# Optimization experiments

Measured on AMD Instinct MI355X. Metric: run time of the kernel, lower is better.

## Reference

```python
import jax, jax.numpy as jnp
import numpy as np
from itertools import combinations

# ---- G(3,0,1) projective geometric algebra tables (blade order: grades 0..4, lexicographic) ----

def _build_tables():
    blades = [c for g in range(5) for c in combinations(range(4), g)]
    index = {b: i for i, b in enumerate(blades)}
    def mul(a, b, e0_sq):
        lst = list(a) + list(b)
        sign = 1
        for i in range(len(lst)):
            for j in range(len(lst) - 1 - i):
                if lst[j] > lst[j + 1]:
                    lst[j], lst[j + 1] = lst[j + 1], lst[j]
                    sign = -sign
        out, i = [], 0
        while i < len(lst):
            if i + 1 < len(lst) and lst[i] == lst[i + 1]:
                if lst[i] == 0:
                    sign *= e0_sq  # e0^2 = 0 in PGA geometric product
                i += 2
            else:
                out.append(lst[i]); i += 1
        return tuple(out), sign
    GP = np.zeros((16, 16, 16), np.float32)
    WEDGE = np.zeros((16, 16, 16), np.float32)
    for a in blades:
        for b in blades:
            bl, s = mul(a, b, 0)
            if s != 0:
                GP[index[a], index[b], index[bl]] += s
            if not (set(a) & set(b)):
                bl, s = mul(a, b, 1)
                WEDGE[index[a], index[b], index[bl]] += s
    D = np.zeros((16, 16), np.float32)
    for a in blades:
        c = tuple(sorted(set(range(4)) - set(a)))
        bl, s = mul(a, c, 1)  # e_a ^ e_c = s * e0123
        D[index[c], index[a]] = s
    Dinv = np.linalg.inv(D).astype(np.float32)
    # 9 Pin(3,0,1)-equivariant linear basis maps: 5 grade projections + 4 left-mult by e0
    B = np.zeros((9, 16, 16), np.float32)
    for i, a in enumerate(blades):
        B[len(a), i, i] = 1.0
        if 0 not in a:
            tgt = tuple(sorted((0,) + a))
            B[5 + len(a), index[tgt], i] = 1.0
    inner_idx = np.array([i for i, a in enumerate(blades) if 0 not in a])  # invariant inner product skips e0 blades
    return (jnp.asarray(GP), jnp.asarray(WEDGE), jnp.asarray(D), jnp.asarray(Dinv), jnp.asarray(B), jnp.asarray(inner_idx))

GP_T, WEDGE_T, DUAL, DUAL_INV, BASIS, INNER_IDX = _build_tables()
N_HEADS = 8  # gatr SelfAttentionConfig default


def equi_linear(x, W):
    # x: [..., in_ch, 16], W: [out_ch, in_ch, 9] -> [..., out_ch, 16]
    return jnp.einsum('...ik,oib,bjk->...oj', x, W, BASIS)


def equi_norm(x, eps=1e-6):
    sq = jnp.sum(jnp.take(x, INNER_IDX, axis=-1) ** 2, axis=-1)      # [..., C]
    factor = jnp.mean(sq, axis=-1, keepdims=True)[..., None]          # [..., 1, 1]
    return x * jax.lax.rsqrt(factor + eps)


def geometric_product(x, y):
    return jnp.einsum('...i,...j,ijk->...k', x, y, GP_T)


def equi_join(x, y):
    xd = jnp.einsum('ji,...i->...j', DUAL, x)
    yd = jnp.einsum('ji,...i->...j', DUAL, y)
    w = jnp.einsum('...i,...j,ijk->...k', xd, yd, WEDGE_T)
    return jnp.einsum('ji,...i->...j', DUAL_INV, w)


def attention(x, Wq, Wk, Wv, Wo):
    Bb, N, C, _ = x.shape
    ch = C // N_HEADS
    def split(h):
        return h.reshape(Bb, N, N_HEADS, ch, 16).transpose(0, 2, 1, 3, 4)  # [B,H,N,ch,16]
    q = split(equi_linear(x, Wq))
    k = split(equi_linear(x, Wk))
    v = split(equi_linear(x, Wv))
    qi = jnp.take(q, INNER_IDX, axis=-1)
    ki = jnp.take(k, INNER_IDX, axis=-1)
    logits = jnp.einsum('bhnck,bhmck->bhnm', qi, ki) / np.float32(np.sqrt(8 * ch))
    att = jax.nn.softmax(logits, axis=-1)
    out = jnp.einsum('bhnm,bhmck->bhnck', att, v)
    out = out.transpose(0, 2, 1, 3, 4).reshape(Bb, N, C, 16)
    return equi_linear(out, Wo)


def geo_mlp(x, Wl, Wr, Wm):
    C = x.shape[-2]
    half = C // 2
    left = equi_linear(x, Wl)
    right = equi_linear(x, Wr)
    gp = geometric_product(left[..., :half, :], right[..., :half, :])
    jn = equi_join(left[..., half:, :], right[..., half:, :])
    h = jnp.concatenate([gp, jn], axis=-2)
    h = h * jax.nn.gelu(h[..., 0:1], approximate=False)  # scalar-gated GELU
    return equi_linear(h, Wm)


def embed_point(p):
    # PGA point: homogeneous trivector, e123 coefficient 1
    z = jnp.zeros(p.shape[:-1] + (16,), p.dtype)
    z = z.at[..., 11].set(p[..., 2])
    z = z.at[..., 12].set(-p[..., 1])
    z = z.at[..., 13].set(p[..., 0])
    z = z.at[..., 14].set(1.0)
    return z


def reference(points, W_in, Wq, Wk, Wv, Wo, Wl, Wr, Wm, W_out):
    x = embed_point(points)[..., None, :]   # [B, N, 1, 16]
    x = equi_linear(x, W_in)                # [B, N, C, 16]
    def block(xc, p):
        wq, wk, wv, wo, wl, wr, wm = p
        xc = xc + attention(equi_norm(xc), wq, wk, wv, wo)
        xc = xc + geo_mlp(equi_norm(xc), wl, wr, wm)
        return xc, None
    x, _ = jax.lax.scan(block, x, (Wq, Wk, Wv, Wo, Wl, Wr, Wm))
    out = equi_linear(x, W_out)             # [B, N, 1, 16]
    return jnp.mean(out[..., 0], axis=(1, 2))  # [B]


def setup_inputs():
    key = jax.random.key(0)
    ks = jax.random.split(key, 12)
    B, N, C, L = 1, 2048, 16, 10
    def w(k, o, i):
        return jax.random.normal(k, (o, i, 9), jnp.float32) / np.float32(np.sqrt(9.0 * i))
    def wl(k, o, i):
        return jax.random.normal(k, (L, o, i, 9), jnp.float32) / np.float32(np.sqrt(9.0 * i))
    return {
        'points': jax.random.normal(ks[0], (B, N, 3), jnp.float32),
        'W_in': w(ks[1], C, 1),
        'Wq': wl(ks[2], C, C), 'Wk': wl(ks[3], C, C), 'Wv': wl(ks[4], C, C),
        'Wo': wl(ks[5], C, C), 'Wl': wl(ks[6], C, C), 'Wr': wl(ks[7], C, C),
        'Wm': wl(ks[8], C, C), 'W_out': w(ks[9], 1, C),
    }
```

## Files before the change

kernel.cpp:

```cpp
#include <hip/hip_runtime.h>
#include <hip/hip_bf16.h>
#include <math.h>

#define NTOK 2048

typedef short short8v __attribute__((ext_vector_type(8)));
typedef short short4v __attribute__((ext_vector_type(4)));
typedef float f32x4 __attribute__((ext_vector_type(4)));
typedef unsigned u32x4 __attribute__((ext_vector_type(4)));

__device__ __forceinline__ unsigned short f2bf(float x){
  unsigned u = __float_as_uint(x);
  u += 0x7fff + ((u>>16)&1);
  return (unsigned short)(u>>16);
}
__device__ __forceinline__ unsigned pack_bf2(float a, float b){
  __hip_bfloat162 h = __float22bfloat162_rn(float2{a,b});
  return *reinterpret_cast<unsigned*>(&h);
}

struct GEnt { unsigned char i, j, k; signed char s; };

constexpr int IDX2MASK[16] = {0,1,2,4,8,3,5,9,6,10,12,7,11,13,14,15};
constexpr int MASK2IDX[16] = {0,1,2,5,3,6,8,11,4,7,9,12,10,13,14,15};

constexpr int rsign(int a, int b){
  int cnt=0;
  for(int i=0;i<4;++i) if((b>>i)&1) for(int j=i+1;j<4;++j) if((a>>j)&1) cnt++;
  return (cnt&1)?-1:1;
}

struct GPTab { GEnt e[192]; };
constexpr GPTab make_gp(){
  GPTab t{}; int n=0;
  for(int ia=0; ia<16; ++ia) for(int ib=0; ib<16; ++ib){
    int a=IDX2MASK[ia], b=IDX2MASK[ib];
    if(a&b&1) continue;
    t.e[n].i=(unsigned char)ia; t.e[n].j=(unsigned char)ib;
    t.e[n].k=(unsigned char)MASK2IDX[a^b]; t.e[n].s=(signed char)rsign(a,b);
    ++n;
  }
  return t;
}
static constexpr GPTab GP_TAB = make_gp();

struct JTab { GEnt e[81]; };
constexpr JTab make_join(){
  JTab t{}; int n=0;
  for(int ia=0; ia<16; ++ia) for(int ib=0; ib<16; ++ib){
    int a=IDX2MASK[ia], b=IDX2MASK[ib];
    if((a|b)!=15) continue;
    int ca=(~a)&15, cb=(~b)&15, k=a&b, ck=(~k)&15;
    int s = rsign(a,ca)*rsign(b,cb)*rsign(ca,cb)*rsign(k,ck);
    t.e[n].i=(unsigned char)ia; t.e[n].j=(unsigned char)ib;
    t.e[n].k=(unsigned char)MASK2IDX[k]; t.e[n].s=(signed char)s;
    ++n;
  }
  return t;
}
static constexpr JTab J_TAB = make_join();

constexpr int INNER[8] = {0,2,3,4,8,9,10,14};

__device__ __forceinline__ void apply_gp(float* o, const float* a, const float* b){
#pragma unroll
  for(int n=0;n<192;++n){
    const float s = (float)GP_TAB.e[n].s;
    o[GP_TAB.e[n].k] = fmaf(s*a[GP_TAB.e[n].i], b[GP_TAB.e[n].j], o[GP_TAB.e[n].k]);
  }
}
__device__ __forceinline__ void apply_join(float* o, const float* a, const float* b){
#pragma unroll
  for(int n=0;n<81;++n){
    const float s = (float)J_TAB.e[n].s;
    o[J_TAB.e[n].k] = fmaf(s*a[J_TAB.e[n].i], b[J_TAB.e[n].j], o[J_TAB.e[n].k]);
  }
}

__device__ __forceinline__ void elin_row(float acc[16], const float* xin, const float* w0p){
#pragma unroll
  for(int j=0;j<16;++j) acc[j]=0.0f;
#pragma unroll
  for(int i=0;i<16;++i){
    const float* w = w0p + i*9;
    const float4* xp = (const float4*)(xin + i*16);
    float4 A=xp[0], B=xp[1], Cc=xp[2], D=xp[3];
    float w0=w[0],w1=w[1],w2=w[2],w3=w[3],w4=w[4],w5=w[5],w6=w[6],w7=w[7],w8=w[8];
    acc[0] = fmaf(w0, A.x,  acc[0]);
    acc[1] = fmaf(w1, A.y,  acc[1]);
    acc[2] = fmaf(w1, A.z,  acc[2]);
    acc[3] = fmaf(w1, A.w,  acc[3]);
    acc[4] = fmaf(w1, B.x,  acc[4]);
    acc[5] = fmaf(w2, B.y,  acc[5]);
    acc[6] = fmaf(w2, B.z,  acc[6]);
    acc[7] = fmaf(w2, B.w,  acc[7]);
    acc[8] = fmaf(w2, Cc.x, acc[8]);
    acc[9] = fmaf(w2, Cc.y, acc[9]);
    acc[10]= fmaf(w2, Cc.z, acc[10]);
    acc[11]= fmaf(w3, Cc.w, acc[11]);
    acc[12]= fmaf(w3, D.x,  acc[12]);
    acc[13]= fmaf(w3, D.y,  acc[13]);
    acc[14]= fmaf(w3, D.z,  acc[14]);
    acc[15]= fmaf(w4, D.w,  acc[15]);
    acc[1] = fmaf(w5, A.x,  acc[1]);
    acc[5] = fmaf(w6, A.z,  acc[5]);
    acc[6] = fmaf(w6, A.w,  acc[6]);
    acc[7] = fmaf(w6, B.x,  acc[7]);
    acc[11]= fmaf(w7, Cc.x, acc[11]);
    acc[12]= fmaf(w7, Cc.y, acc[12]);
    acc[13]= fmaf(w7, Cc.z, acc[13]);
    acc[15]= fmaf(w8, D.z,  acc[15]);
  }
}

__device__ __forceinline__ float gelu_exact(float x){
  return 0.5f*x*(1.0f+erff(x*0.70710678118654752f));
}

#define WPAD 145
#define TBS  264
#define TPB  8

template<int MODE>
__global__ __launch_bounds__(128) void token_kernel(
    const float* __restrict__ points, const float* __restrict__ Win,
    const float* __restrict__ Wo, const float* __restrict__ Wl,
    const float* __restrict__ Wr, const float* __restrict__ Wm,
    const float* __restrict__ Wq, const float* __restrict__ Wk,
    const float* __restrict__ Wv, const float* __restrict__ Wout,
    const float* __restrict__ ATT, float* __restrict__ X,
    unsigned short* __restrict__ Qg16, unsigned short* __restrict__ Kg16,
    unsigned short* __restrict__ VgT, float* __restrict__ toksum)
{
  __shared__ float wlds[6*16*WPAD];
  __shared__ float buf[TPB*TBS];
  __shared__ float sred[TPB*16];
  const int tid = threadIdx.x;
  const int t = tid>>4, o = tid&15;
  const int n = blockIdx.x*TPB + t;

  auto stage = [&](float* dst, const float* src){
#pragma unroll
    for(int r=0;r<18;++r){
      int k = tid + r*128;
      dst[(k/144)*WPAD + (k%144)] = src[k];
    }
  };
  if (MODE==0){ stage(wlds+3*16*WPAD, Wq); stage(wlds+4*16*WPAD, Wk); stage(wlds+5*16*WPAD, Wv); }
  if (MODE==1){ stage(wlds+0*16*WPAD, Wl); stage(wlds+1*16*WPAD, Wr); stage(wlds+2*16*WPAD, Wm);
                stage(wlds+3*16*WPAD, Wq); stage(wlds+4*16*WPAD, Wk); stage(wlds+5*16*WPAD, Wv); }
  if (MODE==2){ stage(wlds+0*16*WPAD, Wl); stage(wlds+1*16*WPAD, Wr); stage(wlds+2*16*WPAD, Wm); }

  float* tb = buf + t*TBS;
  float xr[16];

  if (MODE==0){
    float px = points[n*3+0], py = points[n*3+1], pz = points[n*3+2];
    float w3 = Win[o*9+3], w8 = Win[o*9+8];
#pragma unroll
    for(int j=0;j<16;++j) xr[j]=0.0f;
    xr[11]= w3*pz; xr[12]= -w3*py; xr[13]= w3*px; xr[14]= w3; xr[15]= w8;
    float4* xg = (float4*)(X + (size_t)n*256 + o*16);
    xg[0]=make_float4(xr[0],xr[1],xr[2],xr[3]);
    xg[1]=make_float4(xr[4],xr[5],xr[6],xr[7]);
    xg[2]=make_float4(xr[8],xr[9],xr[10],xr[11]);
    xg[3]=make_float4(xr[12],xr[13],xr[14],xr[15]);
  } else {
    const float4* xg = (const float4*)(X + (size_t)n*256 + o*16);
    float4 a=xg[0],b=xg[1],c=xg[2],d=xg[3];
    xr[0]=a.x; xr[1]=a.y; xr[2]=a.z; xr[3]=a.w;
    xr[4]=b.x; xr[5]=b.y; xr[6]=b.z; xr[7]=b.w;
    xr[8]=c.x; xr[9]=c.y; xr[10]=c.z; xr[11]=c.w;
    xr[12]=d.x; xr[13]=d.y; xr[14]=d.z; xr[15]=d.w;
    const float4* ag = (const float4*)(ATT + (size_t)n*256 + o*16);
    float4* bp = (float4*)(tb + o*16);
    bp[0]=ag[0]; bp[1]=ag[1]; bp[2]=ag[2]; bp[3]=ag[3];
    __syncthreads();
    float acc[16];
    elin_row(acc, tb, Wo + o*144);
#pragma unroll
    for(int j=0;j<16;++j) xr[j]+=acc[j];
    float s=0;
#pragma unroll
    for(int z=0;z<8;++z){ float v=xr[INNER[z]]; s=fmaf(v,v,s); }
    sred[tid]=s; __syncthreads();
    float tot=0;
#pragma unroll
    for(int c2=0;c2<16;++c2) tot += sred[t*16+c2];
    float f = 1.0f/sqrtf(tot*(1.0f/16.0f)+1e-6f);
    float4* bp2=(float4*)(tb+o*16);
    bp2[0]=make_float4(xr[0]*f,xr[1]*f,xr[2]*f,xr[3]*f);
    bp2[1]=make_float4(xr[4]*f,xr[5]*f,xr[6]*f,xr[7]*f);
    bp2[2]=make_float4(xr[8]*f,xr[9]*f,xr[10]*f,xr[11]*f);
    bp2[3]=make_float4(xr[12]*f,xr[13]*f,xr[14]*f,xr[15]*f);
    __syncthreads();
    float L[16], R[16];
    elin_row(L, tb, wlds+0*16*WPAD + o*WPAD);
    elin_row(R, tb, wlds+1*16*WPAD + o*WPAD);
    float h[16];
#pragma unroll
    for(int j=0;j<16;++j) h[j]=0.0f;
    if (o<8) apply_gp(h,L,R); else apply_join(h,L,R);
    float gel = gelu_exact(h[0]);
#pragma unroll
    for(int j=0;j<16;++j) h[j]*=gel;
    __syncthreads();
    float4* bp3=(float4*)(tb+o*16);
    bp3[0]=make_float4(h[0],h[1],h[2],h[3]);
    bp3[1]=make_float4(h[4],h[5],h[6],h[7]);
    bp3[2]=make_float4(h[8],h[9],h[10],h[11]);
    bp3[3]=make_float4(h[12],h[13],h[14],h[15]);
    __syncthreads();
    float mm2[16];
    elin_row(mm2, tb, wlds+2*16*WPAD + o*WPAD);
#pragma unroll
    for(int j=0;j<16;++j) xr[j]+=mm2[j];
    if (MODE==1){
      float4* xs = (float4*)(X + (size_t)n*256 + o*16);
      xs[0]=make_float4(xr[0],xr[1],xr[2],xr[3]);
      xs[1]=make_float4(xr[4],xr[5],xr[6],xr[7]);
      xs[2]=make_float4(xr[8],xr[9],xr[10],xr[11]);
      xs[3]=make_float4(xr[12],xr[13],xr[14],xr[15]);
    }
  }

  if (MODE==2){
    sred[tid] = Wout[o*9]*xr[0];
    __syncthreads();
    if (o==0){
      float s2=0;
#pragma unroll
      for(int c2=0;c2<16;++c2) s2+=sred[t*16+c2];
      toksum[n]=s2;
    }
    return;
  }

  {
    float s=0;
#pragma unroll
    for(int z=0;z<8;++z){ float v=xr[INNER[z]]; s=fmaf(v,v,s); }
    sred[tid]=s; __syncthreads();
    float tot=0;
#pragma unroll
    for(int c2=0;c2<16;++c2) tot += sred[t*16+c2];
    float f2 = 1.0f/sqrtf(tot*(1.0f/16.0f)+1e-6f);
    float4* bp4=(float4*)(tb+o*16);
    bp4[0]=make_float4(xr[0]*f2,xr[1]*f2,xr[2]*f2,xr[3]*f2);
    bp4[1]=make_float4(xr[4]*f2,xr[5]*f2,xr[6]*f2,xr[7]*f2);
    bp4[2]=make_float4(xr[8]*f2,xr[9]*f2,xr[10]*f2,xr[11]*f2);
    bp4[3]=make_float4(xr[12]*f2,xr[13]*f2,xr[14]*f2,xr[15]*f2);
    __syncthreads();
    float q_[16],k_[16],v_[16];
    elin_row(q_, tb, wlds+3*16*WPAD+o*WPAD);
    elin_row(k_, tb, wlds+4*16*WPAD+o*WPAD);
    elin_row(v_, tb, wlds+5*16*WPAD+o*WPAD);
    int hh=o>>1, cc=o&1;
    {
      unsigned qw[4], kw[4];
#pragma unroll
      for(int j=0;j<4;++j){
        unsigned short a0=f2bf(q_[INNER[2*j]]*0.25f), a1=f2bf(q_[INNER[2*j+1]]*0.25f);
        unsigned short b0=f2bf(k_[INNER[2*j]]),       b1=f2bf(k_[INNER[2*j+1]]);
        qw[j] = (unsigned)a0 | ((unsigned)a1<<16);
        kw[j] = (unsigned)b0 | ((unsigned)b1<<16);
      }
      size_t rb = ((size_t)hh*NTOK + n)*16 + cc*8;
      *(uint4*)(Qg16 + rb) = make_uint4(qw[0],qw[1],qw[2],qw[3]);
      *(uint4*)(Kg16 + rb) = make_uint4(kw[0],kw[1],kw[2],kw[3]);
    }
    __syncthreads();
    {
      float4* vb = (float4*)(tb + o*16);
      vb[0]=make_float4(v_[0],v_[1],v_[2],v_[3]);
      vb[1]=make_float4(v_[4],v_[5],v_[6],v_[7]);
      vb[2]=make_float4(v_[8],v_[9],v_[10],v_[11]);
      vb[3]=make_float4(v_[12],v_[13],v_[14],v_[15]);
    }
    __syncthreads();
#pragma unroll
    for(int pp=0;pp<2;++pp){
      int p  = tid + pp*128;
      int h2 = p>>5, v2 = p&31;
      int oc = 2*h2 + (v2>>4), c2 = v2&15;
      unsigned vw[4];
#pragma unroll
      for(int j=0;j<4;++j){
        unsigned short e0=f2bf(buf[(2*j  )*TBS + oc*16 + c2]);
        unsigned short e1=f2bf(buf[(2*j+1)*TBS + oc*16 + c2]);
        vw[j]=(unsigned)e0 | ((unsigned)e1<<16);
      }
      *(uint4*)(VgT + ((size_t)(h2*32+v2))*NTOK + (size_t)blockIdx.x*TPB) = make_uint4(vw[0],vw[1],vw[2],vw[3]);
    }
  }
}

__global__ __launch_bounds__(256) void attn_kernel(
    const unsigned short* __restrict__ Qg16, const unsigned short* __restrict__ Kg16,
    const unsigned short* __restrict__ VgT,  float* __restrict__ ATT)
{
  __shared__ float cmb[4*32*17];
  __shared__ float ml[4*16*2];
  const int tid = threadIdx.x;
  const int l   = tid & 63, w = tid >> 6;
  const int h   = blockIdx.x >> 7, qb = blockIdx.x & 127;
  const int l15 = l & 15, lg = l >> 4;

  const short4v z4 = {0,0,0,0};
  short8v qf;
  {
    const short4v* qp = (const short4v*)(Qg16 + ((size_t)(h*NTOK + qb*16 + l15))*16 + lg*4);
    qf = __builtin_shufflevector(*qp, z4, 0,1,2,3,4,5,6,7);
  }

  const int key0 = w*512;
  const size_t vrow = ((size_t)(h*32 + l15))*NTOK;

  float mx = -INFINITY;
#pragma unroll 2
  for(int kc=0; kc<512; kc+=64){
#pragma unroll
    for(int t2=0;t2<4;++t2){
      const short4v* kp = (const short4v*)(Kg16 + ((size_t)(h*NTOK + key0 + kc + t2*16 + l15))*16 + lg*4);
      short8v kf = __builtin_shufflevector(*kp, z4, 0,1,2,3,4,5,6,7);
      f32x4 z = {0,0,0,0};
      f32x4 S = __builtin_amdgcn_mfma_f32_16x16x32_bf16(kf, qf, z, 0,0,0);
      mx = fmaxf(mx, fmaxf(fmaxf(S[0],S[1]), fmaxf(S[2],S[3])));
    }
  }
  mx = fmaxf(mx, __shfl_xor(mx, 16));
  mx = fmaxf(mx, __shfl_xor(mx, 32));
  const float M = mx;

  f32x4 acc0 = {0,0,0,0}, acc1 = {0,0,0,0};
  float ls = 0.0f;
#pragma unroll 2
  for(int kc=0; kc<512; kc+=64){
    f32x4 S[4];
#pragma unroll
    for(int t2=0;t2<4;++t2){
      const short4v* kp = (const short4v*)(Kg16 + ((size_t)(h*NTOK + key0 + kc + t2*16 + l15))*16 + lg*4);
      short8v kf = __builtin_shufflevector(*kp, z4, 0,1,2,3,4,5,6,7);
      f32x4 z = {0,0,0,0};
      S[t2] = __builtin_amdgcn_mfma_f32_16x16x32_bf16(kf, qf, z, 0,0,0);
    }
    float p[4][4];
#pragma unroll
    for(int t2=0;t2<4;++t2)
#pragma unroll
      for(int r=0;r<4;++r){ float pv = __expf(S[t2][r]-M); p[t2][r]=pv; ls += pv; }
    u32x4 paw, paw2;
    paw[0]=pack_bf2(p[0][0],p[0][1]); paw[1]=pack_bf2(p[0][2],p[0][3]);
    paw[2]=pack_bf2(p[1][0],p[1][1]); paw[3]=pack_bf2(p[1][2],p[1][3]);
    paw2[0]=pack_bf2(p[2][0],p[2][1]); paw2[1]=pack_bf2(p[2][2],p[2][3]);
    paw2[2]=pack_bf2(p[3][0],p[3][1]); paw2[3]=pack_bf2(p[3][2],p[3][3]);
    short8v pa  = *reinterpret_cast<short8v*>(&paw);
    short8v pa2 = *reinterpret_cast<short8v*>(&paw2);
    size_t vb = vrow + key0 + kc;
    const short4v* v0a = (const short4v*)(VgT + vb + lg*4);
    const short4v* v0b = (const short4v*)(VgT + vb + 16 + lg*4);
    const short4v* v0c = (const short4v*)(VgT + vb + 32 + lg*4);
    const short4v* v0d = (const short4v*)(VgT + vb + 48 + lg*4);
    short8v vb0  = __builtin_shufflevector(*v0a, *v0b, 0,1,2,3,4,5,6,7);
    short8v vb0b = __builtin_shufflevector(*v0c, *v0d, 0,1,2,3,4,5,6,7);
    size_t vb1s = vb + (size_t)16*NTOK;
    const short4v* v1a = (const short4v*)(VgT + vb1s + lg*4);
    const short4v* v1b = (const short4v*)(VgT + vb1s + 16 + lg*4);
    const short4v* v1c = (const short4v*)(VgT + vb1s + 32 + lg*4);
    const short4v* v1d = (const short4v*)(VgT + vb1s + 48 + lg*4);
    short8v vb1  = __builtin_shufflevector(*v1a, *v1b, 0,1,2,3,4,5,6,7);
    short8v vb1b = __builtin_shufflevector(*v1c, *v1d, 0,1,2,3,4,5,6,7);
    acc0 = __builtin_amdgcn_mfma_f32_16x16x32_bf16(pa,  vb0,  acc0, 0,0,0);
    acc0 = __builtin_amdgcn_mfma_f32_16x16x32_bf16(pa2, vb0b, acc0, 0,0,0);
    acc1 = __builtin_amdgcn_mfma_f32_16x16x32_bf16(pa,  vb1,  acc1, 0,0,0);
    acc1 = __builtin_amdgcn_mfma_f32_16x16x32_bf16(pa2, vb1b, acc1, 0,0,0);
  }
  ls += __shfl_xor(ls, 16);
  ls += __shfl_xor(ls, 32);

  {
    float* cw = cmb + w*544;
#pragma unroll
    for(int r=0;r<4;++r){
      cw[ l15     *17 + lg*4 + r] = acc0[r];
      cw[(l15+16) *17 + lg*4 + r] = acc1[r];
    }
    if (lg == 0){
      ml[(w*16 + l15)*2]   = M;
      ml[(w*16 + l15)*2+1] = ls;
    }
  }
  __syncthreads();
  {
    int q = tid & 15, v = tid >> 4;
    float Mg = -INFINITY;
#pragma unroll
    for(int w2=0; w2<4; ++w2) Mg = fmaxf(Mg, ml[(w2*16+q)*2]);
    float L=0, a0=0, a1=0;
#pragma unroll
    for(int w2=0; w2<4; ++w2){
      float ww = __expf(ml[(w2*16+q)*2] - Mg);
      L  = fmaf(ml[(w2*16+q)*2+1], ww, L);
      a0 = fmaf(cmb[w2*544 +  v     *17 + q], ww, a0);
      a1 = fmaf(cmb[w2*544 + (v+16) *17 + q], ww, a1);
    }
    float inv = 1.0f/L;
    int n = qb*16 + q;
    ATT[(size_t)n*256 + (size_t)(2*h  )*16 + v] = a0*inv;
    ATT[(size_t)n*256 + (size_t)(2*h+1)*16 + v] = a1*inv;
  }
}

__global__ __launch_bounds__(256) void reduce_kernel(const float* __restrict__ tok, float* __restrict__ out){
  int tid=threadIdx.x;
  float s=0;
  for(int i=tid;i<NTOK;i+=256) s+=tok[i];
#pragma unroll
  for(int off=32;off>0;off>>=1) s += __shfl_down(s,off);
  __shared__ float red[4];
  if((tid&63)==0) red[tid>>6]=s;
  __syncthreads();
  if(tid==0) out[0]=(red[0]+red[1]+red[2]+red[3])*(1.0f/2048.0f);
}

extern "C" void kernel_launch(void* const* d_in, const int* in_sizes, int n_in,
                              void* d_out, int out_size, void* d_ws, size_t ws_size,
                              hipStream_t stream){
  const float* points=(const float*)d_in[0];
  const float* Win=(const float*)d_in[1];
  const float* Wq=(const float*)d_in[2];
  const float* Wk=(const float*)d_in[3];
  const float* Wv=(const float*)d_in[4];
  const float* Wo=(const float*)d_in[5];
  const float* Wl=(const float*)d_in[6];
  const float* Wr=(const float*)d_in[7];
  const float* Wm=(const float*)d_in[8];
  const float* Wout=(const float*)d_in[9];
  float* ws=(float*)d_ws;
  float* X    = ws;
  float* ATT  = ws + 524288;
  unsigned short* Qg16 = (unsigned short*)(ws + 1048576);
  unsigned short* Kg16 = (unsigned short*)(ws + 1179648);
  unsigned short* VgT  = (unsigned short*)(ws + 1310720);
  float* tok  = ws + 1572864;
  float* out=(float*)d_out;

  token_kernel<0><<<256,128,0,stream>>>(points,Win,nullptr,nullptr,nullptr,nullptr,
                                        Wq,Wk,Wv,nullptr,nullptr,X,Qg16,Kg16,VgT,nullptr);
  for(int l=0;l<10;++l){
    attn_kernel<<<1024,256,0,stream>>>(Qg16,Kg16,VgT,ATT);
    if(l<9){
      token_kernel<1><<<256,128,0,stream>>>(nullptr,nullptr,
          Wo+l*2304,Wl+l*2304,Wr+l*2304,Wm+l*2304,
          Wq+(l+1)*2304,Wk+(l+1)*2304,Wv+(l+1)*2304,nullptr,
          ATT,X,Qg16,Kg16,VgT,nullptr);
    } else {
      token_kernel<2><<<256,128,0,stream>>>(nullptr,nullptr,
          Wo+l*2304,Wl+l*2304,Wr+l*2304,Wm+l*2304,
          nullptr,nullptr,nullptr,Wout,
          ATT,X,nullptr,nullptr,nullptr,tok);
    }
  }
  reduce_kernel<<<1,256,0,stream>>>(tok,out);
}
```

Baseline: 692.6 us.

## Split attention keys across eight waves and software-prefetch K/V fragments

The attention kernel now launches 512 threads per block, so eight waves each handle 256 keys instead of four waves handling 512. The shared-memory combine step merges eight partial softmax states, and each thread writes one output element. The second pass also double-buffers the K and V fragment loads one chunk ahead, to hide global-load latency behind the MFMA and exp work. The cost is higher register pressure from the prefetch buffers, larger shared arrays, and redundant Q loads and max passes per wave.

Measured after the change: 775.5 us. +12.0%, slower.

```diff
diff --git a/kernel.cpp b/kernel.cpp
--- a/kernel.cpp
+++ b/kernel.cpp
@@ -295,12 +295,12 @@
   }
 }
 
-__global__ __launch_bounds__(256) void attn_kernel(
+__global__ __launch_bounds__(512, 8) void attn_kernel(
     const unsigned short* __restrict__ Qg16, const unsigned short* __restrict__ Kg16,
     const unsigned short* __restrict__ VgT,  float* __restrict__ ATT)
 {
-  __shared__ float cmb[4*32*17];
-  __shared__ float ml[4*16*2];
+  __shared__ float cmb[8*32*17];
+  __shared__ float ml[8*16*2];
   const int tid = threadIdx.x;
   const int l   = tid & 63, w = tid >> 6;
   const int h   = blockIdx.x >> 7, qb = blockIdx.x & 127;
@@ -313,18 +313,42 @@
     qf = __builtin_shufflevector(*qp, z4, 0,1,2,3,4,5,6,7);
   }
 
-  const int key0 = w*512;
+  const int key0 = w*256;
   const size_t vrow = ((size_t)(h*32 + l15))*NTOK;
 
-  float mx = -INFINITY;
-#pragma unroll 2
-  for(int kc=0; kc<512; kc+=64){
+  auto LOADK = [&](int kc, short8v (&kf)[4]){
 #pragma unroll
     for(int t2=0;t2<4;++t2){
       const short4v* kp = (const short4v*)(Kg16 + ((size_t)(h*NTOK + key0 + kc + t2*16 + l15))*16 + lg*4);
-      short8v kf = __builtin_shufflevector(*kp, z4, 0,1,2,3,4,5,6,7);
+      kf[t2] = __builtin_shufflevector(*kp, z4, 0,1,2,3,4,5,6,7);
+    }
+  };
+  auto LOADV = [&](int kc, short8v (&vf)[4]){
+    size_t vb0 = vrow + key0 + kc;
+    size_t vb1 = vb0 + (size_t)16*NTOK;
+    const short4v* a0 = (const short4v*)(VgT + vb0 + lg*4);
+    const short4v* b0 = (const short4v*)(VgT + vb0 + 16 + lg*4);
+    const short4v* c0 = (const short4v*)(VgT + vb0 + 32 + lg*4);
+    const short4v* d0 = (const short4v*)(VgT + vb0 + 48 + lg*4);
+    vf[0] = __builtin_shufflevector(*a0, *b0, 0,1,2,3,4,5,6,7);
+    vf[1] = __builtin_shufflevector(*c0, *d0, 0,1,2,3,4,5,6,7);
+    const short4v* a1 = (const short4v*)(VgT + vb1 + lg*4);
+    const short4v* b1 = (const short4v*)(VgT + vb1 + 16 + lg*4);
+    const short4v* c1 = (const short4v*)(VgT + vb1 + 32 + lg*4);
+    const short4v* d1 = (const short4v*)(VgT + vb1 + 48 + lg*4);
+    vf[2] = __builtin_shufflevector(*a1, *b1, 0,1,2,3,4,5,6,7);
+    vf[3] = __builtin_shufflevector(*c1, *d1, 0,1,2,3,4,5,6,7);
+  };
+
+  float mx = -INFINITY;
+#pragma unroll
+  for(int kc=0; kc<256; kc+=64){
+    short8v kf[4];
+    LOADK(kc, kf);
+#pragma unroll
+    for(int t2=0;t2<4;++t2){
       f32x4 z = {0,0,0,0};
-      f32x4 S = __builtin_amdgcn_mfma_f32_16x16x32_bf16(kf, qf, z, 0,0,0);
+      f32x4 S = __builtin_amdgcn_mfma_f32_16x16x32_bf16(kf[t2], qf, z, 0,0,0);
       mx = fmaxf(mx, fmaxf(fmaxf(S[0],S[1]), fmaxf(S[2],S[3])));
     }
   }
@@ -334,15 +358,16 @@
 
   f32x4 acc0 = {0,0,0,0}, acc1 = {0,0,0,0};
   float ls = 0.0f;
-#pragma unroll 2
-  for(int kc=0; kc<512; kc+=64){
+  short8v kfc[4], vfc[4], kfn[4], vfn[4];
+  LOADK(0, kfc); LOADV(0, vfc);
+#pragma unroll
+  for(int it=0; it<4; ++it){
+    if (it<3){ LOADK((it+1)*64, kfn); LOADV((it+1)*64, vfn); }
     f32x4 S[4];
 #pragma unroll
     for(int t2=0;t2<4;++t2){
-      const short4v* kp = (const short4v*)(Kg16 + ((size_t)(h*NTOK + key0 + kc + t2*16 + l15))*16 + lg*4);
-      short8v kf = __builtin_shufflevector(*kp, z4, 0,1,2,3,4,5,6,7);
       f32x4 z = {0,0,0,0};
-      S[t2] = __builtin_amdgcn_mfma_f32_16x16x32_bf16(kf, qf, z, 0,0,0);
+      S[t2] = __builtin_amdgcn_mfma_f32_16x16x32_bf16(kfc[t2], qf, z, 0,0,0);
     }
     float p[4][4];
 #pragma unroll
@@ -356,24 +381,12 @@
     paw2[2]=pack_bf2(p[3][0],p[3][1]); paw2[3]=pack_bf2(p[3][2],p[3][3]);
     short8v pa  = *reinterpret_cast<short8v*>(&paw);
     short8v pa2 = *reinterpret_cast<short8v*>(&paw2);
-    size_t vb = vrow + key0 + kc;
-    const short4v* v0a = (const short4v*)(VgT + vb + lg*4);
-    const short4v* v0b = (const short4v*)(VgT + vb + 16 + lg*4);
-    const short4v* v0c = (const short4v*)(VgT + vb + 32 + lg*4);
-    const short4v* v0d = (const short4v*)(VgT + vb + 48 + lg*4);
-    short8v vb0  = __builtin_shufflevector(*v0a, *v0b, 0,1,2,3,4,5,6,7);
-    short8v vb0b = __builtin_shufflevector(*v0c, *v0d, 0,1,2,3,4,5,6,7);
-    size_t vb1s = vb + (size_t)16*NTOK;
-    const short4v* v1a = (const short4v*)(VgT + vb1s + lg*4);
-    const short4v* v1b = (const short4v*)(VgT + vb1s + 16 + lg*4);
-    const short4v* v1c = (const short4v*)(VgT + vb1s + 32 + lg*4);
-    const short4v* v1d = (const short4v*)(VgT + vb1s + 48 + lg*4);
-    short8v vb1  = __builtin_shufflevector(*v1a, *v1b, 0,1,2,3,4,5,6,7);
-    short8v vb1b = __builtin_shufflevector(*v1c, *v1d, 0,1,2,3,4,5,6,7);
-    acc0 = __builtin_amdgcn_mfma_f32_16x16x32_bf16(pa,  vb0,  acc0, 0,0,0);
-    acc0 = __builtin_amdgcn_mfma_f32_16x16x32_bf16(pa2, vb0b, acc0, 0,0,0);
-    acc1 = __builtin_amdgcn_mfma_f32_16x16x32_bf16(pa,  vb1,  acc1, 0,0,0);
-    acc1 = __builtin_amdgcn_mfma_f32_16x16x32_bf16(pa2, vb1b, acc1, 0,0,0);
+    acc0 = __builtin_amdgcn_mfma_f32_16x16x32_bf16(pa,  vfc[0], acc0, 0,0,0);
+    acc0 = __builtin_amdgcn_mfma_f32_16x16x32_bf16(pa2, vfc[1], acc0, 0,0,0);
+    acc1 = __builtin_amdgcn_mfma_f32_16x16x32_bf16(pa,  vfc[2], acc1, 0,0,0);
+    acc1 = __builtin_amdgcn_mfma_f32_16x16x32_bf16(pa2, vfc[3], acc1, 0,0,0);
+#pragma unroll
+    for(int z2=0;z2<4;++z2){ kfc[z2]=kfn[z2]; vfc[z2]=vfn[z2]; }
   }
   ls += __shfl_xor(ls, 16);
   ls += __shfl_xor(ls, 32);
@@ -395,19 +408,16 @@
     int q = tid & 15, v = tid >> 4;
     float Mg = -INFINITY;
 #pragma unroll
-    for(int w2=0; w2<4; ++w2) Mg = fmaxf(Mg, ml[(w2*16+q)*2]);
-    float L=0, a0=0, a1=0;
-#pragma unroll
-    for(int w2=0; w2<4; ++w2){
+    for(int w2=0; w2<8; ++w2) Mg = fmaxf(Mg, ml[(w2*16+q)*2]);
+    float L=0, a=0;
+#pragma unroll
+    for(int w2=0; w2<8; ++w2){
       float ww = __expf(ml[(w2*16+q)*2] - Mg);
-      L  = fmaf(ml[(w2*16+q)*2+1], ww, L);
-      a0 = fmaf(cmb[w2*544 +  v     *17 + q], ww, a0);
-      a1 = fmaf(cmb[w2*544 + (v+16) *17 + q], ww, a1);
-    }
-    float inv = 1.0f/L;
+      L = fmaf(ml[(w2*16+q)*2+1], ww, L);
+      a = fmaf(cmb[w2*544 + v*17 + q], ww, a);
+    }
     int n = qb*16 + q;
-    ATT[(size_t)n*256 + (size_t)(2*h  )*16 + v] = a0*inv;
-    ATT[(size_t)n*256 + (size_t)(2*h+1)*16 + v] = a1*inv;
+    ATT[(size_t)n*256 + (size_t)(2*h + (v>>4))*16 + (v&15)] = a/L;
   }
 }
 
@@ -448,7 +458,7 @@
   token_kernel<0><<<256,128,0,stream>>>(points,Win,nullptr,nullptr,nullptr,nullptr,
                                         Wq,Wk,Wv,nullptr,nullptr,X,Qg16,Kg16,VgT,nullptr);
   for(int l=0;l<10;++l){
-    attn_kernel<<<1024,256,0,stream>>>(Qg16,Kg16,VgT,ATT);
+    attn_kernel<<<1024,512,0,stream>>>(Qg16,Kg16,VgT,ATT);
     if(l<9){
       token_kernel<1><<<256,128,0,stream>>>(nullptr,nullptr,
           Wo+l*2304,Wl+l*2304,Wr+l*2304,Wm+l*2304,
```
